# Performance work log

Hardware: AMD Instinct MI355X
Metric: run time of the kernel (lower is better)

The kernel has to match this reference:

```python
import jax, jax.numpy as jnp
import numpy as np
import math

B, S, D, H = 2, 2048, 1024, 16
DH = D // H


def setup_inputs() -> dict:
    key = jax.random.key(0)
    ks = jax.random.split(key, 10)
    scale = 1.0 / math.sqrt(D)
    inp = {
        "x": jax.random.normal(ks[0], (B, S, D), dtype=jnp.float32),
        "valid_nums": jax.random.randint(ks[1], (B,), 1, S + 1, dtype=jnp.int32),
        "Wq": jax.random.normal(ks[2], (D, D), dtype=jnp.float32) * scale,
        "bq": jnp.zeros((D,), dtype=jnp.float32),
        "Wk": jax.random.normal(ks[3], (D, D), dtype=jnp.float32) * scale,
        "bk": jnp.zeros((D,), dtype=jnp.float32),
        "Wv": jax.random.normal(ks[4], (D, D), dtype=jnp.float32) * scale,
        "bv": jnp.zeros((D,), dtype=jnp.float32),
        "Wo": jax.random.normal(ks[5], (D, D), dtype=jnp.float32) * scale,
        "bo": jnp.zeros((D,), dtype=jnp.float32),
    }
    return inp


def _split_heads(t):
    # (B, S, D) -> (B, H, S, DH)
    return t.reshape(B, S, H, DH).transpose(0, 2, 1, 3)


def reference(x, valid_nums, Wq, bq, Wk, bk, Wv, bv, Wo, bo):
    q = _split_heads(x @ Wq + bq)
    k = _split_heads(x @ Wk + bk)
    v = _split_heads(x @ Wv + bv)
    scores = jnp.einsum("bhqd,bhkd->bhqk", q, k) / math.sqrt(DH)  # (B,H,S,S)
    # length mask over keys: key j valid iff j < valid_nums[b]
    key_mask = jnp.arange(S)[None, :] < valid_nums[:, None]        # (B,S)
    scores = jnp.where(key_mask[:, None, None, :], scores, -jnp.inf)
    attn = jax.nn.softmax(scores, axis=-1)
    out = jnp.einsum("bhqk,bhkd->bhqd", attn, v)                   # (B,H,S,DH)
    out = out.transpose(0, 2, 1, 3).reshape(B, S, D)
    return out @ Wo + bo
```

## Files before the change

kernel.cpp:

```cpp
#include <hip/hip_runtime.h>
#include <hip/hip_bf16.h>
#include <math.h>

static constexpr int Bb = 2, Ss = 2048, Dd = 1024, Hh = 16, DHh = 64;
static constexpr int Mm = Bb * Ss;
static constexpr int Kk = Dd;

typedef __attribute__((ext_vector_type(8))) short bf16x8;
typedef __attribute__((ext_vector_type(4))) float f32x4;
typedef unsigned short us;

__device__ inline short f2b(float f) {
    __hip_bfloat16 h = __float2bfloat16(f);
    return *reinterpret_cast<short*>(&h);
}
__device__ inline float b2f(us u) {
    __hip_bfloat16 h = *reinterpret_cast<__hip_bfloat16*>(&u);
    return __bfloat162float(h);
}
__device__ inline unsigned pk2(float lo, float hi) {
    return ((unsigned)(us)f2b(hi) << 16) | (unsigned)(us)f2b(lo);
}

__device__ inline void gload16(us* lds, const us* g) {
    __builtin_amdgcn_global_load_lds(
        (const __attribute__((address_space(1))) void*)g,
        (__attribute__((address_space(3))) void*)lds,
        16, 0, 0);
}

__global__ __launch_bounds__(256)
void xconv_kernel(const float* __restrict__ x, us* __restrict__ xb)
{
    const size_t i = ((size_t)blockIdx.x * 256 + threadIdx.x) * 8;
    float4 a = *(const float4*)(x + i);
    float4 b = *(const float4*)(x + i + 4);
    bf16x8 t;
    t[0] = f2b(a.x); t[1] = f2b(a.y); t[2] = f2b(a.z); t[3] = f2b(a.w);
    t[4] = f2b(b.x); t[5] = f2b(b.y); t[6] = f2b(b.z); t[7] = f2b(b.w);
    *(bf16x8*)(xb + i) = t;
}

__global__ __launch_bounds__(256)
void wtrans_kernel(const float* __restrict__ Wq, const float* __restrict__ Wk,
                   const float* __restrict__ Wv, const float* __restrict__ Wo,
                   us* __restrict__ Wt, us* __restrict__ Woth, us* __restrict__ Wotl)
{
    __shared__ float T[64][65];
    const int z = blockIdx.z;
    const float* W = (z == 0) ? Wq : (z == 1) ? Wk : (z == 2) ? Wv : Wo;
    const int split = (z == 3);
    us* dh = split ? Woth : (Wt + (size_t)z * Dd * Kk);
    us* dl = Wotl;

    const int n0 = blockIdx.x * 64, k0 = blockIdx.y * 64;
    const int tid = threadIdx.x;
    const int r = tid >> 2, c0 = (tid & 3) * 16;
#pragma unroll
    for (int j = 0; j < 4; ++j) {
        float4 v = *(const float4*)(W + (size_t)(k0 + r) * Dd + n0 + c0 + 4 * j);
        T[r][c0 + 4 * j + 0] = v.x;
        T[r][c0 + 4 * j + 1] = v.y;
        T[r][c0 + 4 * j + 2] = v.z;
        T[r][c0 + 4 * j + 3] = v.w;
    }
    __syncthreads();
    us hi[16], lo[16];
#pragma unroll
    for (int j = 0; j < 16; ++j) {
        float v = T[c0 + j][r];
        us h = (us)f2b(v);
        hi[j] = h;
        if (split) lo[j] = (us)f2b(v - b2f(h));
    }
    *(bf16x8*)&dh[(size_t)(n0 + r) * Kk + k0 + c0]     = *(bf16x8*)&hi[0];
    *(bf16x8*)&dh[(size_t)(n0 + r) * Kk + k0 + c0 + 8] = *(bf16x8*)&hi[8];
    if (split) {
        *(bf16x8*)&dl[(size_t)(n0 + r) * Kk + k0 + c0]     = *(bf16x8*)&lo[0];
        *(bf16x8*)&dl[(size_t)(n0 + r) * Kk + k0 + c0 + 8] = *(bf16x8*)&lo[8];
    }
}

__global__ __launch_bounds__(256)
void gemm_qkv_kernel(const us* __restrict__ xb, const us* __restrict__ Wt,
                     const float* __restrict__ bq, const float* __restrict__ bk,
                     const float* __restrict__ bv, us* __restrict__ QKV)
{
    __shared__ us As[128 * 64];
    __shared__ us Bs[128 * 64];
    const int tid = threadIdx.x;
    const int wave = tid >> 6, lane = tid & 63;
    const int wr = wave >> 1, wc = wave & 1;
    const int lg = lane >> 4, ll = lane & 15;
    const int col0 = blockIdx.x * 128;
    const int row0 = blockIdx.y * 128;

    f32x4 acc[4][4];
#pragma unroll
    for (int mt = 0; mt < 4; ++mt)
#pragma unroll
        for (int nt = 0; nt < 4; ++nt)
#pragma unroll
            for (int r = 0; r < 4; ++r) acc[mt][nt][r] = 0.f;

    const us* Ag = xb + (size_t)(row0 + wave * 32 + (lane >> 3)) * Kk + (lane & 7) * 8;
    const us* Bg = Wt + (size_t)(col0 + wave * 32 + (lane >> 3)) * Kk + (lane & 7) * 8;
    us* Ad = &As[(wave * 4) * 512];
    us* Bd = &Bs[(wave * 4) * 512];

    for (int k0 = 0; k0 < Kk; k0 += 64) {
        __syncthreads();
#pragma unroll
        for (int i = 0; i < 4; ++i) {
            gload16(Ad + i * 512, Ag + (size_t)(i * 8) * Kk + k0);
            gload16(Bd + i * 512, Bg + (size_t)(i * 8) * Kk + k0);
        }
        __syncthreads();
#pragma unroll
        for (int ks = 0; ks < 2; ++ks) {
            bf16x8 af[4], bfr[4];
#pragma unroll
            for (int mt = 0; mt < 4; ++mt)
                af[mt] = *(const bf16x8*)&As[(wr * 64 + mt * 16 + ll) * 64 + ks * 32 + lg * 8];
#pragma unroll
            for (int nt = 0; nt < 4; ++nt)
                bfr[nt] = *(const bf16x8*)&Bs[(wc * 64 + nt * 16 + ll) * 64 + ks * 32 + lg * 8];
#pragma unroll
            for (int mt = 0; mt < 4; ++mt)
#pragma unroll
                for (int nt = 0; nt < 4; ++nt)
                    acc[mt][nt] = __builtin_amdgcn_mfma_f32_16x16x32_bf16(af[mt], bfr[nt], acc[mt][nt], 0, 0, 0);
        }
    }

    const int z = col0 >> 10;
    const int c0 = col0 & 1023;
    const float* bias = (z == 0) ? bq : (z == 1) ? bk : bv;
    const float osc = (z == 0) ? 0.125f : 1.0f;
    us* outz = QKV + (size_t)z * Mm * Dd;

    if (z == 2) {
#pragma unroll
        for (int mt = 0; mt < 4; ++mt)
#pragma unroll
            for (int nt = 0; nt < 4; ++nt) {
                int row = row0 + wr * 64 + mt * 16 + lg * 4;
                int col = c0 + wc * 64 + nt * 16 + ll;
                int b_ = row >> 11, s_ = row & 2047;
                float bv_ = bias[col];
                union { us u[4]; uint2 d2; } pk;
#pragma unroll
                for (int r = 0; r < 4; ++r) pk.u[r] = (us)f2b(acc[mt][nt][r] + bv_);
                *(uint2*)&outz[((size_t)(b_ * Hh * DHh) + col) * Ss + s_] = pk.d2;
            }
    } else {
#pragma unroll
        for (int mt = 0; mt < 4; ++mt)
#pragma unroll
            for (int nt = 0; nt < 4; ++nt)
#pragma unroll
                for (int r = 0; r < 4; ++r) {
                    int row = row0 + wr * 64 + mt * 16 + lg * 4 + r;
                    int col = c0 + wc * 64 + nt * 16 + ll;
                    float v = (acc[mt][nt][r] + bias[col]) * osc;
                    int b_ = row >> 11, s_ = row & 2047, h_ = col >> 6, d_ = col & 63;
                    outz[(((size_t)(b_ * Hh + h_)) * Ss + s_) * DHh + d_] = (us)f2b(v);
                }
    }
}

__global__ __launch_bounds__(256)
void gemm_final_kernel(const us* __restrict__ Oh, const us* __restrict__ Ol,
                       const us* __restrict__ Wth, const us* __restrict__ Wtl,
                       const float* __restrict__ bo, float* __restrict__ out)
{
    __shared__ us AhS[128 * 64];
    __shared__ us AlS[128 * 64];
    __shared__ us BhS[64 * 64];
    __shared__ us BlS[64 * 64];
    const int tid = threadIdx.x;
    const int wave = tid >> 6, lane = tid & 63;
    const int wr = wave >> 1, wc = wave & 1;
    const int lg = lane >> 4, ll = lane & 15;
    const int col0 = blockIdx.x * 64;
    const int row0 = blockIdx.y * 128;

    f32x4 acc[4][2];
#pragma unroll
    for (int mt = 0; mt < 4; ++mt)
#pragma unroll
        for (int nt = 0; nt < 2; ++nt)
#pragma unroll
            for (int r = 0; r < 4; ++r) acc[mt][nt][r] = 0.f;

    const size_t aoff = (size_t)(row0 + wave * 32 + (lane >> 3)) * Kk + (lane & 7) * 8;
    const size_t boff = (size_t)(col0 + wave * 16 + (lane >> 3)) * Kk + (lane & 7) * 8;
    const us* Ahg = Oh + aoff;
    const us* Alg = Ol + aoff;
    const us* Bhg = Wth + boff;
    const us* Blg = Wtl + boff;
    us* AhD = &AhS[(wave * 4) * 512];
    us* AlD = &AlS[(wave * 4) * 512];
    us* BhD = &BhS[(wave * 2) * 512];
    us* BlD = &BlS[(wave * 2) * 512];

    for (int k0 = 0; k0 < Kk; k0 += 64) {
        __syncthreads();
#pragma unroll
        for (int i = 0; i < 4; ++i) {
            gload16(AhD + i * 512, Ahg + (size_t)(i * 8) * Kk + k0);
            gload16(AlD + i * 512, Alg + (size_t)(i * 8) * Kk + k0);
        }
#pragma unroll
        for (int j = 0; j < 2; ++j) {
            gload16(BhD + j * 512, Bhg + (size_t)(j * 8) * Kk + k0);
            gload16(BlD + j * 512, Blg + (size_t)(j * 8) * Kk + k0);
        }
        __syncthreads();
#pragma unroll
        for (int ks = 0; ks < 2; ++ks) {
            bf16x8 ah[4], al[4], bh[2], bl[2];
#pragma unroll
            for (int mt = 0; mt < 4; ++mt) {
                ah[mt] = *(const bf16x8*)&AhS[(wr * 64 + mt * 16 + ll) * 64 + ks * 32 + lg * 8];
                al[mt] = *(const bf16x8*)&AlS[(wr * 64 + mt * 16 + ll) * 64 + ks * 32 + lg * 8];
            }
#pragma unroll
            for (int nt = 0; nt < 2; ++nt) {
                bh[nt] = *(const bf16x8*)&BhS[(wc * 32 + nt * 16 + ll) * 64 + ks * 32 + lg * 8];
                bl[nt] = *(const bf16x8*)&BlS[(wc * 32 + nt * 16 + ll) * 64 + ks * 32 + lg * 8];
            }
#pragma unroll
            for (int mt = 0; mt < 4; ++mt)
#pragma unroll
                for (int nt = 0; nt < 2; ++nt) {
                    acc[mt][nt] = __builtin_amdgcn_mfma_f32_16x16x32_bf16(ah[mt], bh[nt], acc[mt][nt], 0, 0, 0);
                    acc[mt][nt] = __builtin_amdgcn_mfma_f32_16x16x32_bf16(al[mt], bh[nt], acc[mt][nt], 0, 0, 0);
                    acc[mt][nt] = __builtin_amdgcn_mfma_f32_16x16x32_bf16(ah[mt], bl[nt], acc[mt][nt], 0, 0, 0);
                }
        }
    }

#pragma unroll
    for (int mt = 0; mt < 4; ++mt)
#pragma unroll
        for (int nt = 0; nt < 2; ++nt)
#pragma unroll
            for (int r = 0; r < 4; ++r) {
                int row = row0 + wr * 64 + mt * 16 + lg * 4 + r;
                int col = col0 + wc * 32 + nt * 16 + ll;
                out[(size_t)row * Dd + col] = acc[mt][nt][r] + bo[col];
            }
}

__global__ __launch_bounds__(256)
void attn_mfma_kernel(const us* __restrict__ Q, const us* __restrict__ K,
                      const us* __restrict__ Vt_g, const int* __restrict__ valid_nums,
                      us* __restrict__ Oh, us* __restrict__ Ol)
{
    const int bh = blockIdx.y;
    const int b  = bh >> 4, h = bh & 15;
    const int q0 = blockIdx.x * 64;
    const int tid  = threadIdx.x;
    const int wave = tid >> 6;
    const int lane = tid & 63;
    const int lg = lane >> 4;
    const int ll = lane & 15;

    const int nv = valid_nums[b];
    const int ntiles = (nv + 63) >> 6;

    const us* Qb = Q    + (size_t)bh * Ss * DHh;
    const us* Kb = K    + (size_t)bh * Ss * DHh;
    const us* Vb = Vt_g + (size_t)bh * DHh * Ss;

    __shared__ us Ks[64][68];
    __shared__ us Vs[64][68];

    bf16x8 qa[2];
    {
        const us* qrow = Qb + (size_t)(q0 + wave * 16 + ll) * DHh;
        qa[0] = *(const bf16x8*)(qrow + lg * 8);
        qa[1] = *(const bf16x8*)(qrow + 32 + lg * 8);
    }

    union { unsigned w[4]; bf16x8 v; } ones_u;
#pragma unroll
    for (int i = 0; i < 4; ++i) ones_u.w[i] = 0x3F803F80u;
    const bf16x8 vones = ones_u.v;

    f32x4 o[4], o4;
#pragma unroll
    for (int nt = 0; nt < 4; ++nt) { o[nt][0]=0.f; o[nt][1]=0.f; o[nt][2]=0.f; o[nt][3]=0.f; }
    o4[0]=0.f; o4[1]=0.f; o4[2]=0.f; o4[3]=0.f;
    float mq = -INFINITY;

    const int srow = tid >> 2;
    const int scol = (tid & 3) * 16;

    for (int kt = 0; kt < ntiles; ++kt) {
        const int k0 = kt * 64;
        __syncthreads();
        {
            const us* Kr = Kb + (size_t)(k0 + srow) * DHh + scol;
            *(bf16x8*)&Ks[srow][scol]     = *(const bf16x8*)Kr;
            *(bf16x8*)&Ks[srow][scol + 8] = *(const bf16x8*)(Kr + 8);
            const us* Vr = Vb + (size_t)srow * Ss + k0 + scol;
            *(bf16x8*)&Vs[srow][scol]     = *(const bf16x8*)Vr;
            *(bf16x8*)&Vs[srow][scol + 8] = *(const bf16x8*)(Vr + 8);
        }
        __syncthreads();

        f32x4 s[4];
#pragma unroll
        for (int nt = 0; nt < 4; ++nt) { s[nt][0]=0.f; s[nt][1]=0.f; s[nt][2]=0.f; s[nt][3]=0.f; }
#pragma unroll
        for (int ks = 0; ks < 2; ++ks) {
#pragma unroll
            for (int nt = 0; nt < 4; ++nt) {
                bf16x8 kf = *(const bf16x8*)&Ks[nt * 16 + ll][ks * 32 + lg * 8];
                s[nt] = __builtin_amdgcn_mfma_f32_16x16x32_bf16(kf, qa[ks], s[nt], 0, 0, 0);
            }
        }

        float p[4][4];
        float mx;
        if (k0 + 64 <= nv) {
#pragma unroll
            for (int nt = 0; nt < 4; ++nt)
#pragma unroll
                for (int r = 0; r < 4; ++r) p[nt][r] = s[nt][r];
            mx = fmaxf(fmaxf(fmaxf(p[0][0], p[0][1]), fmaxf(p[0][2], p[0][3])),
                       fmaxf(fmaxf(p[1][0], p[1][1]), fmaxf(p[1][2], p[1][3])));
            mx = fmaxf(mx,
                 fmaxf(fmaxf(fmaxf(p[2][0], p[2][1]), fmaxf(p[2][2], p[2][3])),
                       fmaxf(fmaxf(p[3][0], p[3][1]), fmaxf(p[3][2], p[3][3]))));
        } else {
            mx = -INFINITY;
#pragma unroll
            for (int nt = 0; nt < 4; ++nt)
#pragma unroll
                for (int r = 0; r < 4; ++r) {
                    int key = k0 + nt * 16 + lg * 4 + r;
                    float v = (key < nv) ? s[nt][r] : -INFINITY;
                    p[nt][r] = v;
                    mx = fmaxf(mx, v);
                }
        }
        mx = fmaxf(mx, __shfl_xor(mx, 16));
        mx = fmaxf(mx, __shfl_xor(mx, 32));

        const bool rescale = !__all(mx <= mq + 8.f);
        if (rescale) {
            float mn = fmaxf(mq, mx);
            float corr = __expf(mq - mn);
            mq = mn;
            float corr4[4];
#pragma unroll
            for (int r = 0; r < 4; ++r) corr4[r] = __shfl(corr, lg * 16 + lg * 4 + r);
#pragma unroll
            for (int nt = 0; nt < 4; ++nt)
#pragma unroll
                for (int r = 0; r < 4; ++r) o[nt][r] *= corr4[r];
#pragma unroll
            for (int r = 0; r < 4; ++r) o4[r] *= corr4[r];
        }

#pragma unroll
        for (int nt = 0; nt < 4; ++nt)
#pragma unroll
            for (int r = 0; r < 4; ++r) p[nt][r] = __expf(p[nt][r] - mq);

        unsigned dw[4][2];
#pragma unroll
        for (int nt = 0; nt < 4; ++nt) {
            dw[nt][0] = pk2(p[nt][0], p[nt][1]);
            dw[nt][1] = pk2(p[nt][2], p[nt][3]);
        }

        const int sA = ((2 * lg) & 3) * 16 + ll;
        const int sB = ((2 * lg + 1) & 3) * 16 + ll;
        const bool hi = (lg & 2);
#pragma unroll
        for (int ks = 0; ks < 2; ++ks) {
            unsigned a0 = (unsigned)__shfl((int)dw[2 * ks][0],     sA);
            unsigned a1 = (unsigned)__shfl((int)dw[2 * ks][1],     sA);
            unsigned a2 = (unsigned)__shfl((int)dw[2 * ks][0],     sB);
            unsigned a3 = (unsigned)__shfl((int)dw[2 * ks][1],     sB);
            unsigned b0 = (unsigned)__shfl((int)dw[2 * ks + 1][0], sA);
            unsigned b1 = (unsigned)__shfl((int)dw[2 * ks + 1][1], sA);
            unsigned b2 = (unsigned)__shfl((int)dw[2 * ks + 1][0], sB);
            unsigned b3 = (unsigned)__shfl((int)dw[2 * ks + 1][1], sB);
            union { unsigned w[4]; bf16x8 v; } pa;
            pa.w[0] = hi ? b0 : a0;
            pa.w[1] = hi ? b1 : a1;
            pa.w[2] = hi ? b2 : a2;
            pa.w[3] = hi ? b3 : a3;
#pragma unroll
            for (int nt = 0; nt < 4; ++nt) {
                bf16x8 vb = *(const bf16x8*)&Vs[nt * 16 + ll][ks * 32 + lg * 8];
                o[nt] = __builtin_amdgcn_mfma_f32_16x16x32_bf16(pa.v, vb, o[nt], 0, 0, 0);
            }
            o4 = __builtin_amdgcn_mfma_f32_16x16x32_bf16(pa.v, vones, o4, 0, 0, 0);
        }
    }

#pragma unroll
    for (int r = 0; r < 4; ++r) {
        int row = q0 + wave * 16 + lg * 4 + r;
        float linv = 1.f / o4[r];
#pragma unroll
        for (int nt = 0; nt < 4; ++nt) {
            float val = o[nt][r] * linv;
            us uh = (us)f2b(val);
            float rem = val - b2f(uh);
            size_t base = ((size_t)b * Ss + row) * Dd + h * DHh + nt * 16 + ll;
            Oh[base] = uh;
            Ol[base] = (us)f2b(rem);
        }
    }
}

extern "C" void kernel_launch(void* const* d_in, const int* in_sizes, int n_in,
                              void* d_out, int out_size, void* d_ws, size_t ws_size,
                              hipStream_t stream) {
    const float* x     = (const float*)d_in[0];
    const int*   valid = (const int*)d_in[1];
    const float* Wq = (const float*)d_in[2];
    const float* bq = (const float*)d_in[3];
    const float* Wk = (const float*)d_in[4];
    const float* bk = (const float*)d_in[5];
    const float* Wv = (const float*)d_in[6];
    const float* bv = (const float*)d_in[7];
    const float* Wo = (const float*)d_in[8];
    const float* bo = (const float*)d_in[9];

    const size_t per = (size_t)Mm * Dd;
    const size_t wsz = (size_t)Dd * Kk;
    us* wsp  = (us*)d_ws;
    us* QKV  = wsp;
    us* Wt   = QKV + 3 * per;
    us* OhB  = Wt + 3 * wsz;
    us* OlB  = OhB + per;
    us* Woth = OlB + per;
    us* Wotl = Woth + wsz;
    us* xb   = Wotl + wsz;

    xconv_kernel<<<(Mm * Kk) / (256 * 8), 256, 0, stream>>>(x, xb);

    wtrans_kernel<<<dim3(Dd / 64, Kk / 64, 4), 256, 0, stream>>>(
        Wq, Wk, Wv, Wo, Wt, Woth, Wotl);

    gemm_qkv_kernel<<<dim3(3 * Dd / 128, Mm / 128), 256, 0, stream>>>(
        xb, Wt, bq, bk, bv, QKV);

    attn_mfma_kernel<<<dim3(Ss / 64, Bb * Hh), 256, 0, stream>>>(
        QKV, QKV + per, QKV + 2 * per, valid, OhB, OlB);

    gemm_final_kernel<<<dim3(Dd / 64, Mm / 128), 256, 0, stream>>>(
        OhB, OlB, Woth, Wotl, bo, (float*)d_out);
}
```

Measured before the change: 155.1 us.

## Enlarge attention blocks, prefetch K/V tiles, remap grid per XCD, use exp2

Attention blocks grow to 512 threads covering 128 queries, so each K/V tile loaded into LDS serves twice as many queries. The next tile's K/V is prefetched into registers while the current tile is computed. A flat grid is remapped so blocks of the same batch-head land on the same XCD, which should improve L2 reuse. The log2(e) factor is folded into the Q scale so the kernel can call native exp2, and the rescale threshold is adjusted to match the base-2 domain. The trade-off is fewer blocks in the grid and a larger per-block footprint.

```diff
diff --git a/kernel.cpp b/kernel.cpp
--- a/kernel.cpp
+++ b/kernel.cpp
@@ -20,6 +20,9 @@
 }
 __device__ inline unsigned pk2(float lo, float hi) {
     return ((unsigned)(us)f2b(hi) << 16) | (unsigned)(us)f2b(lo);
+}
+__device__ inline float ex2(float x) {
+    return __builtin_amdgcn_exp2f(x);
 }
 
 __device__ inline void gload16(us* lds, const us* g) {
@@ -136,7 +139,7 @@
     const int z = col0 >> 10;
     const int c0 = col0 & 1023;
     const float* bias = (z == 0) ? bq : (z == 1) ? bk : bv;
-    const float osc = (z == 0) ? 0.125f : 1.0f;
+    const float osc = (z == 0) ? 0.125f * 1.44269504f : 1.0f;
     us* outz = QKV + (size_t)z * Mm * Dd;
 
     if (z == 2) {
@@ -253,14 +256,18 @@
             }
 }
 
-__global__ __launch_bounds__(256)
+__global__ __launch_bounds__(512)
 void attn_mfma_kernel(const us* __restrict__ Q, const us* __restrict__ K,
                       const us* __restrict__ Vt_g, const int* __restrict__ valid_nums,
                       us* __restrict__ Oh, us* __restrict__ Ol)
 {
-    const int bh = blockIdx.y;
-    const int b  = bh >> 4, h = bh & 15;
-    const int q0 = blockIdx.x * 64;
+    const int id  = blockIdx.x;
+    const int xcd = id & 7, grp = id >> 3;
+    const int bh  = (grp >> 4) * 8 + xcd;
+    const int qb  = grp & 15;
+    const int b   = bh >> 4, h = bh & 15;
+    const int q0  = qb * 128;
+
     const int tid  = threadIdx.x;
     const int wave = tid >> 6;
     const int lane = tid & 63;
@@ -295,21 +302,22 @@
     o4[0]=0.f; o4[1]=0.f; o4[2]=0.f; o4[3]=0.f;
     float mq = -INFINITY;
 
-    const int srow = tid >> 2;
-    const int scol = (tid & 3) * 16;
+    const int srow = tid >> 3;
+    const int scol = (tid & 7) * 8;
+
+    bf16x8 kreg = *(const bf16x8*)(Kb + (size_t)srow * DHh + scol);
+    bf16x8 vreg = *(const bf16x8*)(Vb + (size_t)srow * Ss + scol);
 
     for (int kt = 0; kt < ntiles; ++kt) {
         const int k0 = kt * 64;
         __syncthreads();
-        {
-            const us* Kr = Kb + (size_t)(k0 + srow) * DHh + scol;
-            *(bf16x8*)&Ks[srow][scol]     = *(const bf16x8*)Kr;
-            *(bf16x8*)&Ks[srow][scol + 8] = *(const bf16x8*)(Kr + 8);
-            const us* Vr = Vb + (size_t)srow * Ss + k0 + scol;
-            *(bf16x8*)&Vs[srow][scol]     = *(const bf16x8*)Vr;
-            *(bf16x8*)&Vs[srow][scol + 8] = *(const bf16x8*)(Vr + 8);
-        }
-        __syncthreads();
+        *(bf16x8*)&Ks[srow][scol] = kreg;
+        *(bf16x8*)&Vs[srow][scol] = vreg;
+        __syncthreads();
+        if (kt + 1 < ntiles) {
+            kreg = *(const bf16x8*)(Kb + (size_t)(k0 + 64 + srow) * DHh + scol);
+            vreg = *(const bf16x8*)(Vb + (size_t)srow * Ss + k0 + 64 + scol);
+        }
 
         f32x4 s[4];
 #pragma unroll
@@ -350,10 +358,10 @@
         mx = fmaxf(mx, __shfl_xor(mx, 16));
         mx = fmaxf(mx, __shfl_xor(mx, 32));
 
-        const bool rescale = !__all(mx <= mq + 8.f);
+        const bool rescale = !__all(mx <= mq + 11.5f);
         if (rescale) {
             float mn = fmaxf(mq, mx);
-            float corr = __expf(mq - mn);
+            float corr = ex2(mq - mn);
             mq = mn;
             float corr4[4];
 #pragma unroll
@@ -369,7 +377,7 @@
 #pragma unroll
         for (int nt = 0; nt < 4; ++nt)
 #pragma unroll
-            for (int r = 0; r < 4; ++r) p[nt][r] = __expf(p[nt][r] - mq);
+            for (int r = 0; r < 4; ++r) p[nt][r] = ex2(p[nt][r] - mq);
 
         unsigned dw[4][2];
 #pragma unroll
@@ -454,7 +462,7 @@
     gemm_qkv_kernel<<<dim3(3 * Dd / 128, Mm / 128), 256, 0, stream>>>(
         xb, Wt, bq, bk, bv, QKV);
 
-    attn_mfma_kernel<<<dim3(Ss / 64, Bb * Hh), 256, 0, stream>>>(
+    attn_mfma_kernel<<<(Ss / 128) * (Bb * Hh), 512, 0, stream>>>(
         QKV, QKV + per, QKV + 2 * per, valid, OhB, OlB);
 
     gemm_final_kernel<<<dim3(Dd / 64, Mm / 128), 256, 0, stream>>>(
```

New measurement: 145.8 us. -6.1%, faster.
